# Kernel optimization log

Hardware: AMD Instinct MI355X
Metric: run time of the kernel (lower is better)

The kernel has to match this reference:

```python
import jax, jax.numpy as jnp
import numpy as np

N_NODES = 100000
N_EDGES = 1600000
IN_FEAT = 128
UNITS = 64


def setup_inputs() -> dict:
    key = jax.random.key(0)
    k1, k2, k3, k4, k5 = jax.random.split(key, 5)
    node_states = jax.random.normal(k1, (N_NODES, IN_FEAT), dtype=jnp.float32)
    # edges[:,0] is the destination/segment id; the original TF code's
    # repeat(bincount) normalization assumes edges sorted by edges[:,0].
    dst = jnp.sort(jax.random.randint(k2, (N_EDGES,), 0, N_NODES))
    src = jax.random.randint(k3, (N_EDGES,), 0, N_NODES)
    edges = jnp.stack([dst, src], axis=1).astype(jnp.int64)
    kernel = jax.random.normal(k4, (IN_FEAT, UNITS), dtype=jnp.float32) * 0.05
    kernel_attention = jax.random.normal(k5, (2 * UNITS, 1), dtype=jnp.float32) * 0.05
    return {"node_states": node_states, "edges": edges,
            "kernel": kernel, "kernel_attention": kernel_attention}


def reference(node_states, edges, kernel, kernel_attention):
    n_nodes = node_states.shape[0]
    dst = edges[:, 0]  # segment ids (aggregation target)
    src = edges[:, 1]  # neighbor being gathered

    h = node_states @ kernel                      # [N, U]
    h_dst = h[dst]                                # [E, U]
    h_src = h[src]                                # [E, U]
    # concat(h_dst, h_src) @ a  ==  h_dst @ a[:U] + h_src @ a[U:]
    u = kernel_attention.shape[0] // 2
    scores = (h_dst @ kernel_attention[:u] + h_src @ kernel_attention[u:])[:, 0]  # [E]
    scores = jax.nn.leaky_relu(scores, negative_slope=0.2)  # tf default alpha=0.2
    scores = jnp.exp(jnp.clip(scores, -2.0, 2.0))

    score_sum = jax.ops.segment_sum(scores, dst, num_segments=n_nodes)  # [N]
    attn = scores / score_sum[dst]                                      # [E]

    out = jax.ops.segment_sum(h_src * attn[:, None], dst, num_segments=n_nodes)  # [N, U]
    return out
```

## Files before the change

kernel.cpp:

```cpp
#include <hip/hip_runtime.h>
#include <hip/hip_bf16.h>

#define NN 100000
#define NE 1600000
#define NF 128
#define UU 64

typedef __attribute__((ext_vector_type(8))) short short8;
typedef __attribute__((ext_vector_type(4))) float f32x4;

static const size_t OFF_FLAG = 0;
static const size_t OFF_SRC  = 256;
static const size_t OFF_H2   = OFF_SRC + (size_t)NE * 4;
static const size_t OFF_AD   = OFF_H2  + (size_t)NN * UU * 2;
static const size_t OFF_AS   = OFF_AD  + (size_t)NN * 4;
static const size_t OFF_ROW  = OFF_AS  + (size_t)NN * 4;
static const size_t OFF_WP   = OFF_ROW + (size_t)(NN + 1) * 4;

__device__ __forceinline__ unsigned short bfr(float v) {
    unsigned u = __float_as_uint(v);
    return (unsigned short)((u + 0x7FFFu + ((u >> 16) & 1u)) >> 16);
}

__global__ __launch_bounds__(256) void prep(const int* __restrict__ ew,
                                            const float* __restrict__ W,
                                            int* __restrict__ flag,
                                            unsigned short* __restrict__ Wp) {
    if (blockIdx.x == 0) {
        if (threadIdx.x == 0) {
            int a = ew[2 * 400000 + 1] | ew[2 * 800000 + 1] |
                    ew[2 * 1200000 + 1] | ew[2 * 1599999 + 1];
            *flag = (a == 0) ? 1 : 0;
        }
        return;
    }
    int i = (blockIdx.x - 1) * 256 + threadIdx.x;
    int j   = i & 7;
    int l15 = (i >> 3) & 15;
    int quad = (i >> 7) & 3;
    int kb  = (i >> 9) & 3;
    int nt  = i >> 11;
    Wp[i] = bfr(W[(size_t)(kb * 32 + quad * 8 + j) * UU + nt * 16 + l15]);
}

#define GEMM_BLOCKS   1563
#define ROWS_BLOCKS   391
#define UNPACK_BLOCKS 1563

__global__ __launch_bounds__(256) void mega(const float* __restrict__ X,
                                            const void* __restrict__ edges,
                                            const int* __restrict__ flag,
                                            const unsigned short* __restrict__ Wp,
                                            const float* __restrict__ ka,
                                            unsigned short* __restrict__ h2,
                                            float* __restrict__ a_dst,
                                            float* __restrict__ a_src,
                                            int* __restrict__ src32,
                                            int* __restrict__ rows) {
    int bid = blockIdx.x;
    int tid = threadIdx.x;

    if (bid < GEMM_BLOCKS) {
        int wv = tid >> 6, lane = tid & 63;
        int quad = lane >> 4, l15 = lane & 15;
        int nb = bid * 64 + wv * 16;
        int row = nb + l15; if (row >= NN) row = NN - 1;
        const float* xr = X + (size_t)row * NF + quad * 8;

        short8 afrag[4];
#pragma unroll
        for (int kb = 0; kb < 4; kb++) {
            float4 p0 = *(const float4*)(xr + kb * 32);
            float4 p1 = *(const float4*)(xr + kb * 32 + 4);
            short8 a;
            a[0] = (short)bfr(p0.x); a[1] = (short)bfr(p0.y);
            a[2] = (short)bfr(p0.z); a[3] = (short)bfr(p0.w);
            a[4] = (short)bfr(p1.x); a[5] = (short)bfr(p1.y);
            a[6] = (short)bfr(p1.z); a[7] = (short)bfr(p1.w);
            afrag[kb] = a;
        }

        f32x4 acc[4] = {f32x4{0,0,0,0}, f32x4{0,0,0,0}, f32x4{0,0,0,0}, f32x4{0,0,0,0}};
        const short8* wpf = (const short8*)Wp;
#pragma unroll
        for (int nt = 0; nt < 4; nt++) {
#pragma unroll
            for (int kb = 0; kb < 4; kb++) {
                short8 b = wpf[((nt * 4 + kb) * 4 + quad) * 16 + l15];
                acc[nt] = __builtin_amdgcn_mfma_f32_16x16x32_bf16(afrag[kb], b, acc[nt], 0, 0, 0);
            }
        }

        float kad[4], kas[4];
#pragma unroll
        for (int nt = 0; nt < 4; nt++) {
            kad[nt] = ka[nt * 16 + l15];
            kas[nt] = ka[64 + nt * 16 + l15];
        }
#pragma unroll
        for (int r = 0; r < 4; r++) {
            int m = nb + quad * 4 + r;
            if (m < NN) {
#pragma unroll
                for (int nt = 0; nt < 4; nt++)
                    h2[(size_t)m * UU + nt * 16 + l15] = bfr(acc[nt][r]);
            }
            float pd = acc[0][r] * kad[0] + acc[1][r] * kad[1] + acc[2][r] * kad[2] + acc[3][r] * kad[3];
            float ps = acc[0][r] * kas[0] + acc[1][r] * kas[1] + acc[2][r] * kas[2] + acc[3][r] * kas[3];
            pd += __shfl_xor(pd, 1); pd += __shfl_xor(pd, 2);
            pd += __shfl_xor(pd, 4); pd += __shfl_xor(pd, 8);
            ps += __shfl_xor(ps, 1); ps += __shfl_xor(ps, 2);
            ps += __shfl_xor(ps, 4); ps += __shfl_xor(ps, 8);
            if (l15 == 0 && m < NN) { a_dst[m] = pd; a_src[m] = ps; }
        }
        return;
    }
    bid -= GEMM_BLOCKS;

    if (bid < ROWS_BLOCKS) {
        int n = bid * 256 + tid;
        if (n > NN) return;
        if (n == NN) { rows[NN] = NE; return; }
        int fl = *flag;
        const int* ew = (const int*)edges;
        int lo = 0, hi = NE;
        while (lo < hi) {
            int mid = (lo + hi) >> 1;
            int d = fl ? ew[4 * (size_t)mid] : ew[2 * (size_t)mid];
            if (d < n) lo = mid + 1; else hi = mid;
        }
        rows[n] = lo;
        return;
    }
    bid -= ROWS_BLOCKS;

    {
        int fl = *flag;
        if (fl) {
            const int4* ev = (const int4*)edges;
#pragma unroll
            for (int t = 0; t < 4; t++) {
                int i = bid * 1024 + t * 256 + tid;
                if (i < NE) { int4 v = ev[i]; src32[i] = v.z; }
            }
        } else {
            const int4* ev = (const int4*)edges;
#pragma unroll
            for (int t = 0; t < 2; t++) {
                int p = bid * 512 + t * 256 + tid;
                if (p * 2 < NE) {
                    int4 v = ev[p];
                    *(int2*)(src32 + p * 2) = make_int2(v.y, v.w);
                }
            }
        }
    }
}

__device__ __forceinline__ float edge_score(float ad, float as) {
    float sc = ad + as;
    sc = sc > 0.f ? sc : 0.2f * sc;
    sc = fminf(fmaxf(sc, -2.f), 2.f);
    return __expf(sc);
}

__global__ __launch_bounds__(256) void aggregate(const int* __restrict__ rows,
                                                 const int* __restrict__ srcv,
                                                 const unsigned short* __restrict__ h2,
                                                 const float* __restrict__ a_dst,
                                                 const float* __restrict__ a_src,
                                                 float* __restrict__ out) {
    int gid = blockIdx.x * blockDim.x + threadIdx.x;
    int n = gid >> 6;
    int lane = gid & 63;
    if (n >= NN) return;
    int s = rows[n], e = rows[n + 1];
    int cnt = e - s;
    float ad = a_dst[n];
    int g = lane >> 4, gl = lane & 15;
    const unsigned short* h2g = h2 + gl * 4;
    float4 acc = make_float4(0.f, 0.f, 0.f, 0.f);

#define GBATCH(C0, N)                                                            \
    {                                                                            \
        uint2 rr[4]; float sw[4]; int sjv[4];                                    \
        _Pragma("unroll")                                                        \
        for (int t = 0; t < (N); t++) {                                          \
            int j = (C0) + t * 4 + g;                                            \
            sjv[t] = __shfl(mysrc, j);                                           \
            sw[t]  = __shfl(myscore, j);                                         \
        }                                                                        \
        _Pragma("unroll")                                                        \
        for (int t = 0; t < (N); t++)                                            \
            rr[t] = *(const uint2*)(h2g + (size_t)sjv[t] * UU);                  \
        _Pragma("unroll")                                                        \
        for (int t = 0; t < (N); t++) {                                          \
            acc.x += sw[t] * __uint_as_float(rr[t].x << 16);                     \
            acc.y += sw[t] * __uint_as_float(rr[t].x & 0xFFFF0000u);             \
            acc.z += sw[t] * __uint_as_float(rr[t].y << 16);                     \
            acc.w += sw[t] * __uint_as_float(rr[t].y & 0xFFFF0000u);             \
        }                                                                        \
    }

    float inv;
    if (cnt <= 64) {
        int idx = s + lane;
        int mysrc = 0; float myscore = 0.f;
        if (idx < e) { mysrc = srcv[idx]; myscore = edge_score(ad, a_src[mysrc]); }
        int c = 0;
        for (; c + 16 <= cnt; c += 16) GBATCH(c, 4);
        int rem = cnt - c;
        if (rem > 12)     GBATCH(c, 4)
        else if (rem > 8) GBATCH(c, 3)
        else if (rem > 4) GBATCH(c, 2)
        else if (rem > 0) GBATCH(c, 1);
        float t = myscore;
#pragma unroll
        for (int off = 32; off; off >>= 1) t += __shfl_xor(t, off);
        inv = (cnt > 0) ? 1.f / t : 0.f;
    } else {
        float ssum = 0.f;
        for (int i = s + lane; i < e; i += 64) ssum += edge_score(ad, a_src[srcv[i]]);
#pragma unroll
        for (int off = 32; off; off >>= 1) ssum += __shfl_xor(ssum, off);
        inv = 1.f / ssum;
        for (int c0 = s; c0 < e; c0 += 64) {
            int i = c0 + lane;
            int mysrc = 0; float myscore = 0.f;
            if (i < e) { mysrc = srcv[i]; myscore = edge_score(ad, a_src[mysrc]); }
            GBATCH(0, 4); GBATCH(16, 4); GBATCH(32, 4); GBATCH(48, 4);
        }
    }
#undef GBATCH

    acc.x += __shfl_xor(acc.x, 32); acc.y += __shfl_xor(acc.y, 32);
    acc.z += __shfl_xor(acc.z, 32); acc.w += __shfl_xor(acc.w, 32);
    acc.x += __shfl_xor(acc.x, 16); acc.y += __shfl_xor(acc.y, 16);
    acc.z += __shfl_xor(acc.z, 16); acc.w += __shfl_xor(acc.w, 16);
    if (lane < 16) {
        float4 o = make_float4(acc.x * inv, acc.y * inv, acc.z * inv, acc.w * inv);
        *(float4*)(out + (size_t)n * UU + gl * 4) = o;
    }
}

extern "C" void kernel_launch(void* const* d_in, const int* in_sizes, int n_in,
                              void* d_out, int out_size, void* d_ws, size_t ws_size,
                              hipStream_t stream) {
    const float* X  = (const float*)d_in[0];
    const void*  Ed = d_in[1];
    const float* W  = (const float*)d_in[2];
    const float* KA = (const float*)d_in[3];
    float* out = (float*)d_out;

    char* ws = (char*)d_ws;
    int*            flag  = (int*)(ws + OFF_FLAG);
    int*            src32 = (int*)(ws + OFF_SRC);
    unsigned short* h2    = (unsigned short*)(ws + OFF_H2);
    float*          a_dst = (float*)(ws + OFF_AD);
    float*          a_src = (float*)(ws + OFF_AS);
    int*            rows  = (int*)(ws + OFF_ROW);
    unsigned short* Wp    = (unsigned short*)(ws + OFF_WP);

    prep<<<33, 256, 0, stream>>>((const int*)Ed, W, flag, Wp);
    mega<<<GEMM_BLOCKS + ROWS_BLOCKS + UNPACK_BLOCKS, 256, 0, stream>>>(
        X, Ed, flag, Wp, KA, h2, a_dst, a_src, src32, rows);
    aggregate<<<(NN * 64 + 255) / 256, 256, 0, stream>>>(rows, src32, h2, a_dst, a_src, out);
}
```

Measured before the change: 160.1 us.

## Precompute per-edge attention weights in separate kernel before aggregation

The edge unpack step moves out of the fused mega kernel into a new kernel that runs after the GEMM. For each edge it computes the exp-clipped leaky-relu score from a_dst and a_src and stores (src, weight) pairs. The aggregate kernel then reads these pairs directly instead of gathering a_src and computing scores itself, which removes a dependent random load from its critical path. In exchange it adds a kernel launch, serializes the unpack behind the GEMM, and doubles the per-edge workspace traffic.

```diff
diff --git a/kernel.cpp b/kernel.cpp
--- a/kernel.cpp
+++ b/kernel.cpp
@@ -10,8 +10,8 @@
 typedef __attribute__((ext_vector_type(4))) float f32x4;
 
 static const size_t OFF_FLAG = 0;
-static const size_t OFF_SRC  = 256;
-static const size_t OFF_H2   = OFF_SRC + (size_t)NE * 4;
+static const size_t OFF_EW   = 256;
+static const size_t OFF_H2   = OFF_EW  + (size_t)NE * 8;
 static const size_t OFF_AD   = OFF_H2  + (size_t)NN * UU * 2;
 static const size_t OFF_AS   = OFF_AD  + (size_t)NN * 4;
 static const size_t OFF_ROW  = OFF_AS  + (size_t)NN * 4;
@@ -45,7 +45,6 @@
 
 #define GEMM_BLOCKS   1563
 #define ROWS_BLOCKS   391
-#define UNPACK_BLOCKS 1563
 
 __global__ __launch_bounds__(256) void mega(const float* __restrict__ X,
                                             const void* __restrict__ edges,
@@ -55,7 +54,6 @@
                                             unsigned short* __restrict__ h2,
                                             float* __restrict__ a_dst,
                                             float* __restrict__ a_src,
-                                            int* __restrict__ src32,
                                             int* __restrict__ rows) {
     int bid = blockIdx.x;
     int tid = threadIdx.x;
@@ -117,7 +115,7 @@
     }
     bid -= GEMM_BLOCKS;
 
-    if (bid < ROWS_BLOCKS) {
+    {
         int n = bid * 256 + tid;
         if (n > NN) return;
         if (n == NN) { rows[NN] = NE; return; }
@@ -130,30 +128,6 @@
             if (d < n) lo = mid + 1; else hi = mid;
         }
         rows[n] = lo;
-        return;
-    }
-    bid -= ROWS_BLOCKS;
-
-    {
-        int fl = *flag;
-        if (fl) {
-            const int4* ev = (const int4*)edges;
-#pragma unroll
-            for (int t = 0; t < 4; t++) {
-                int i = bid * 1024 + t * 256 + tid;
-                if (i < NE) { int4 v = ev[i]; src32[i] = v.z; }
-            }
-        } else {
-            const int4* ev = (const int4*)edges;
-#pragma unroll
-            for (int t = 0; t < 2; t++) {
-                int p = bid * 512 + t * 256 + tid;
-                if (p * 2 < NE) {
-                    int4 v = ev[p];
-                    *(int2*)(src32 + p * 2) = make_int2(v.y, v.w);
-                }
-            }
-        }
     }
 }
 
@@ -164,11 +138,43 @@
     return __expf(sc);
 }
 
+__global__ __launch_bounds__(256) void wkern(const void* __restrict__ edges,
+                                             const int* __restrict__ flag,
+                                             const float* __restrict__ a_dst,
+                                             const float* __restrict__ a_src,
+                                             int2* __restrict__ ew8) {
+    int fl = *flag;
+    int tid = threadIdx.x;
+    if (fl) {
+        const int4* ev = (const int4*)edges;
+#pragma unroll
+        for (int t = 0; t < 4; t++) {
+            int i = blockIdx.x * 1024 + t * 256 + tid;
+            if (i < NE) {
+                int4 v = ev[i];
+                float w = edge_score(a_dst[v.x], a_src[v.z]);
+                ew8[i] = make_int2(v.z, __float_as_int(w));
+            }
+        }
+    } else {
+        const int4* ev = (const int4*)edges;
+#pragma unroll
+        for (int t = 0; t < 2; t++) {
+            int p = blockIdx.x * 512 + t * 256 + tid;
+            if (p * 2 < NE) {
+                int4 v = ev[p];
+                float w0 = edge_score(a_dst[v.x], a_src[v.y]);
+                float w1 = edge_score(a_dst[v.z], a_src[v.w]);
+                int4 o = make_int4(v.y, __float_as_int(w0), v.w, __float_as_int(w1));
+                *(int4*)(ew8 + p * 2) = o;
+            }
+        }
+    }
+}
+
 __global__ __launch_bounds__(256) void aggregate(const int* __restrict__ rows,
-                                                 const int* __restrict__ srcv,
+                                                 const int2* __restrict__ ew8,
                                                  const unsigned short* __restrict__ h2,
-                                                 const float* __restrict__ a_dst,
-                                                 const float* __restrict__ a_src,
                                                  float* __restrict__ out) {
     int gid = blockIdx.x * blockDim.x + threadIdx.x;
     int n = gid >> 6;
@@ -176,7 +182,6 @@
     if (n >= NN) return;
     int s = rows[n], e = rows[n + 1];
     int cnt = e - s;
-    float ad = a_dst[n];
     int g = lane >> 4, gl = lane & 15;
     const unsigned short* h2g = h2 + gl * 4;
     float4 acc = make_float4(0.f, 0.f, 0.f, 0.f);
@@ -188,7 +193,7 @@
         for (int t = 0; t < (N); t++) {                                          \
             int j = (C0) + t * 4 + g;                                            \
             sjv[t] = __shfl(mysrc, j);                                           \
-            sw[t]  = __shfl(myscore, j);                                         \
+            sw[t]  = __shfl(myw, j);                                             \
         }                                                                        \
         _Pragma("unroll")                                                        \
         for (int t = 0; t < (N); t++)                                            \
@@ -205,8 +210,8 @@
     float inv;
     if (cnt <= 64) {
         int idx = s + lane;
-        int mysrc = 0; float myscore = 0.f;
-        if (idx < e) { mysrc = srcv[idx]; myscore = edge_score(ad, a_src[mysrc]); }
+        int mysrc = 0; float myw = 0.f;
+        if (idx < e) { int2 p = ew8[idx]; mysrc = p.x; myw = __int_as_float(p.y); }
         int c = 0;
         for (; c + 16 <= cnt; c += 16) GBATCH(c, 4);
         int rem = cnt - c;
@@ -214,20 +219,20 @@
         else if (rem > 8) GBATCH(c, 3)
         else if (rem > 4) GBATCH(c, 2)
         else if (rem > 0) GBATCH(c, 1);
-        float t = myscore;
+        float t = myw;
 #pragma unroll
         for (int off = 32; off; off >>= 1) t += __shfl_xor(t, off);
         inv = (cnt > 0) ? 1.f / t : 0.f;
     } else {
         float ssum = 0.f;
-        for (int i = s + lane; i < e; i += 64) ssum += edge_score(ad, a_src[srcv[i]]);
+        for (int i = s + lane; i < e; i += 64) ssum += __int_as_float(ew8[i].y);
 #pragma unroll
         for (int off = 32; off; off >>= 1) ssum += __shfl_xor(ssum, off);
         inv = 1.f / ssum;
         for (int c0 = s; c0 < e; c0 += 64) {
             int i = c0 + lane;
-            int mysrc = 0; float myscore = 0.f;
-            if (i < e) { mysrc = srcv[i]; myscore = edge_score(ad, a_src[mysrc]); }
+            int mysrc = 0; float myw = 0.f;
+            if (i < e) { int2 p = ew8[i]; mysrc = p.x; myw = __int_as_float(p.y); }
             GBATCH(0, 4); GBATCH(16, 4); GBATCH(32, 4); GBATCH(48, 4);
         }
     }
@@ -254,7 +259,7 @@
 
     char* ws = (char*)d_ws;
     int*            flag  = (int*)(ws + OFF_FLAG);
-    int*            src32 = (int*)(ws + OFF_SRC);
+    int2*           ew8   = (int2*)(ws + OFF_EW);
     unsigned short* h2    = (unsigned short*)(ws + OFF_H2);
     float*          a_dst = (float*)(ws + OFF_AD);
     float*          a_src = (float*)(ws + OFF_AS);
@@ -262,7 +267,8 @@
     unsigned short* Wp    = (unsigned short*)(ws + OFF_WP);
 
     prep<<<33, 256, 0, stream>>>((const int*)Ed, W, flag, Wp);
-    mega<<<GEMM_BLOCKS + ROWS_BLOCKS + UNPACK_BLOCKS, 256, 0, stream>>>(
-        X, Ed, flag, Wp, KA, h2, a_dst, a_src, src32, rows);
-    aggregate<<<(NN * 64 + 255) / 256, 256, 0, stream>>>(rows, src32, h2, a_dst, a_src, out);
-}
+    mega<<<GEMM_BLOCKS + ROWS_BLOCKS, 256, 0, stream>>>(
+        X, Ed, flag, Wp, KA, h2, a_dst, a_src, rows);
+    wkern<<<1563, 256, 0, stream>>>(Ed, flag, a_dst, a_src, ew8);
+    aggregate<<<(NN * 64 + 255) / 256, 256, 0, stream>>>(rows, ew8, h2, out);
+}
```

Result: no change. 157.6 us (-1.5%).
